# Optimization experiments

Measured on AMD Instinct MI355X. Metric: run time of the kernel, lower is better.

Reference implementation:

```python
import jax, jax.numpy as jnp
import numpy as np

SUBDIVISIONS = 3  # init_kwargs
EPS = 1e-6


def setup_inputs() -> dict:
    key = jax.random.key(0)
    k1, k2, k3 = jax.random.split(key, 3)
    V, K, F = 100000, 32, 64
    features = jax.random.normal(k1, (V, F), dtype=jnp.float32)
    distsq = jax.random.uniform(k2, (V, K), dtype=jnp.float32)
    neighbour_indices = jax.random.randint(k3, (V, K), 0, V, dtype=jnp.int32)
    length_scale = jnp.float32(1.0)  # non-trainable Variable, init 1.0
    return {"features": features, "distsq": distsq,
            "neighbour_indices": neighbour_indices, "length_scale": length_scale}


def reference(features, distsq, neighbour_indices, length_scale):
    # Inference path: no length-scale EMA update (training=None -> in_train_phase takes the
    # unchanged value), distsq is stop-gradient.
    distsq = jax.lax.stop_gradient(distsq)
    scaler = 10.0 * length_scale * float(SUBDIVISIONS)
    d = jnp.sqrt(distsq + EPS)                      # (V, K) neighbor distances
    nfeat = features[neighbour_indices]             # (V, K, F) gathered neighbor features
    outs = []
    for i in range(SUBDIVISIONS):
        offset = float(i) / length_scale            # radius-bin center
        w = jnp.exp(-scaler * (d - offset) ** 2)    # (V, K) Gaussian radius-bin weights
        num = jnp.einsum('vk,vkf->vf', w, nfeat)    # weighted sum over neighbors
        den = jnp.sum(w, axis=1, keepdims=True) + EPS
        outs.append(num / den)                      # soft-pixel weighted mean
    return jnp.concatenate(outs, axis=1)            # (V, SUBDIVISIONS * F)
```

## Files before the change

kernel.cpp:

```cpp
#include <hip/hip_runtime.h>

#define SP_EPS 1e-6f
typedef __fp16 h2 __attribute__((ext_vector_type(2)));
typedef float f32x2 __attribute__((ext_vector_type(2)));

struct __align__(16) QEntry { f32x2 a;  f32x2 b; };

__device__ __forceinline__ f32x2 shflx2(f32x2 x, int m) {
    f32x2 r;
    r.x = __shfl_xor(x.x, m, 64);
    r.y = __shfl_xor(x.y, m, 64);
    return r;
}

__global__ __launch_bounds__(256) void f32_to_f16_kernel(
    const float* __restrict__ in, unsigned* __restrict__ outh, int n4)
{
    int i = blockIdx.x * 256 + threadIdx.x;
    if (i >= n4) return;
    const float4 v = ((const float4*)in)[i];
    h2 p0 = __builtin_amdgcn_cvt_pkrtz(v.x, v.y);
    h2 p1 = __builtin_amdgcn_cvt_pkrtz(v.z, v.w);
    uint2 o;
    o.x = *(unsigned*)&p0;
    o.y = *(unsigned*)&p1;
    ((uint2*)outh)[i] = o;
}

__global__ __launch_bounds__(256) void softpixel_qw_kernel(
    const unsigned short* __restrict__ fb,
    const float* __restrict__ distsq,
    const int*   __restrict__ nidx,
    const float* __restrict__ ls_ptr,
    float*       __restrict__ out,
    int V)
{
    __shared__ QEntry qbuf[4][32];
    const int lane = threadIdx.x & 63;
    const int wv   = threadIdx.x >> 6;
    const int v    = blockIdx.x * 4 + wv;
    const int q    = lane >> 4;
    const int j    = lane & 15;
    const int j32  = lane & 31;
    const int vc   = v < V ? v : V - 1;

    const float ls     = ls_ptr[0];
    const float scaler = 30.0f * ls;
    const float inv_ls = 1.0f / ls;

    const unsigned dvoff = (unsigned)vc * 32u + (unsigned)j32;
    const float dsq = distsq[dvoff];
    const int   nb  = nidx[dvoff];
    const float d   = sqrtf(dsq + SP_EPS);
    const float t1  = d - inv_ls;
    const float t2  = d - 2.0f * inv_ls;
    const float w0  = __expf(-scaler * d  * d);
    const float w1  = __expf(-scaler * t1 * t1);
    const float w2  = __expf(-scaler * t2 * t2);
    if (lane < 32) {
        QEntry e;
        e.a = (f32x2){w0, __int_as_float(nb)};
        e.b = (f32x2){w1, w2};
        qbuf[wv][j32] = e;
    }
    __syncthreads();

    f32x2 a01_0 = {0.f, 0.f}, a23_0 = {0.f, 0.f};
    f32x2 a01_1 = {0.f, 0.f}, a23_1 = {0.f, 0.f};
    f32x2 a01_2 = {0.f, 0.f}, a23_2 = {0.f, 0.f};
    const unsigned j8 = (unsigned)(j << 3);

    #pragma unroll
    for (int kk = 0; kk < 8; ++kk) {
        const QEntry e = qbuf[wv][4 * kk + q];
        const int ik = __float_as_int(e.a.y);
        const unsigned boff = ((unsigned)ik << 7) + j8;
        const uint2 fp = *(const uint2*)((const char*)fb + boff);
        h2 pa, pb;
        *(unsigned*)&pa = fp.x;
        *(unsigned*)&pb = fp.y;
        f32x2 f01; f01.x = (float)pa[0]; f01.y = (float)pa[1];
        f32x2 f23; f23.x = (float)pb[0]; f23.y = (float)pb[1];
        asm("v_pk_fma_f32 %0, %1, %2, %0 op_sel:[0,0,0] op_sel_hi:[0,1,1]"
            : "+v"(a01_0) : "v"(e.a), "v"(f01));
        asm("v_pk_fma_f32 %0, %1, %2, %0 op_sel:[0,0,0] op_sel_hi:[0,1,1]"
            : "+v"(a23_0) : "v"(e.a), "v"(f23));
        asm("v_pk_fma_f32 %0, %1, %2, %0 op_sel:[0,0,0] op_sel_hi:[0,1,1]"
            : "+v"(a01_1) : "v"(e.b), "v"(f01));
        asm("v_pk_fma_f32 %0, %1, %2, %0 op_sel:[0,0,0] op_sel_hi:[0,1,1]"
            : "+v"(a23_1) : "v"(e.b), "v"(f23));
        asm("v_pk_fma_f32 %0, %1, %2, %0 op_sel:[1,0,0] op_sel_hi:[1,1,1]"
            : "+v"(a01_2) : "v"(e.b), "v"(f01));
        asm("v_pk_fma_f32 %0, %1, %2, %0 op_sel:[1,0,0] op_sel_hi:[1,1,1]"
            : "+v"(a23_2) : "v"(e.b), "v"(f23));
    }

    float s0 = w0, s1 = w1, s2 = w2;
    #pragma unroll
    for (int st = 1; st < 32; st <<= 1) {
        s0 += __shfl_xor(s0, st, 64);
        s1 += __shfl_xor(s1, st, 64);
        s2 += __shfl_xor(s2, st, 64);
    }
    const float r0 = __builtin_amdgcn_rcpf(s0 + SP_EPS);
    const float r1 = __builtin_amdgcn_rcpf(s1 + SP_EPS);
    const float r2 = __builtin_amdgcn_rcpf(s2 + SP_EPS);

    a01_0 += shflx2(a01_0, 16);  a01_0 += shflx2(a01_0, 32);
    a23_0 += shflx2(a23_0, 16);  a23_0 += shflx2(a23_0, 32);
    a01_1 += shflx2(a01_1, 16);  a01_1 += shflx2(a01_1, 32);
    a23_1 += shflx2(a23_1, 16);  a23_1 += shflx2(a23_1, 32);
    a01_2 += shflx2(a01_2, 16);  a01_2 += shflx2(a01_2, 32);
    a23_2 += shflx2(a23_2, 16);  a23_2 += shflx2(a23_2, 32);

    if (v < V && q < 3) {
        f32x2 o01, o23;
        float r;
        if (q == 0)      { o01 = a01_0; o23 = a23_0; r = r0; }
        else if (q == 1) { o01 = a01_1; o23 = a23_1; r = r1; }
        else             { o01 = a01_2; o23 = a23_2; r = r2; }
        float4 ov = make_float4(o01.x * r, o01.y * r, o23.x * r, o23.y * r);
        *(float4*)(out + (unsigned)v * 192u + (unsigned)(q << 6) + (unsigned)(j << 2)) = ov;
    }
}

__global__ __launch_bounds__(256) void softpixel_f32_kernel(
    const float* __restrict__ feat,
    const float* __restrict__ distsq,
    const int*   __restrict__ nidx,
    const float* __restrict__ ls_ptr,
    float*       __restrict__ out,
    int V)
{
    const int lane = threadIdx.x & 63;
    const int wv   = threadIdx.x >> 6;
    const int v    = blockIdx.x * 4 + wv;
    if (v >= V) return;

    const float ls     = ls_ptr[0];
    const float scaler = 30.0f * ls;
    const float inv_ls = 1.0f / ls;

    float w0 = 0.f, w1 = 0.f, w2 = 0.f;
    int nb = 0;
    if (lane < 32) {
        const float dsq = distsq[v * 32 + lane];
        nb = nidx[v * 32 + lane];
        const float d  = sqrtf(dsq + SP_EPS);
        const float t1 = d - inv_ls;
        const float t2 = d - 2.0f * inv_ls;
        w0 = __expf(-scaler * d  * d);
        w1 = __expf(-scaler * t1 * t1);
        w2 = __expf(-scaler * t2 * t2);
    }

    float a0 = 0.f, a1 = 0.f, a2 = 0.f;
    float s0 = SP_EPS, s1 = SP_EPS, s2 = SP_EPS;
    #pragma unroll
    for (int k = 0; k < 32; ++k) {
        const int   ik = __shfl(nb, k, 64);
        const float u0 = __shfl(w0, k, 64);
        const float u1 = __shfl(w1, k, 64);
        const float u2 = __shfl(w2, k, 64);
        const float f  = feat[(size_t)ik * 64 + lane];
        a0 = fmaf(u0, f, a0);
        a1 = fmaf(u1, f, a1);
        a2 = fmaf(u2, f, a2);
        s0 += u0; s1 += u1; s2 += u2;
    }
    float* o = out + (size_t)v * 192 + lane;
    o[0]   = a0 / s0;
    o[64]  = a1 / s1;
    o[128] = a2 / s2;
}

extern "C" void kernel_launch(void* const* d_in, const int* in_sizes, int n_in,
                              void* d_out, int out_size, void* d_ws, size_t ws_size,
                              hipStream_t stream) {
    const float* feat   = (const float*)d_in[0];
    const float* distsq = (const float*)d_in[1];
    const int*   nidx   = (const int*)d_in[2];
    const float* ls     = (const float*)d_in[3];

    const int V = in_sizes[1] / 32;
    const int F = in_sizes[0] / V;
    float* out = (float*)d_out;

    const size_t need = (size_t)V * F * sizeof(unsigned short);
    const int grid = (V + 3) / 4;

    if ((size_t)ws_size >= need && F == 64) {
        unsigned* fh = (unsigned*)d_ws;
        const int n4 = V * F / 4;
        f32_to_f16_kernel<<<(n4 + 255) / 256, 256, 0, stream>>>(feat, fh, n4);
        softpixel_qw_kernel<<<grid, 256, 0, stream>>>(
            (const unsigned short*)fh, distsq, nidx, ls, out, V);
    } else {
        softpixel_f32_kernel<<<grid, 256, 0, stream>>>(feat, distsq, nidx, ls, out, V);
    }
}
```

Measured before the change: 74.58 us.

## Process two vertices per wave and replace block barrier with wave barrier

Each 64-lane wave now handles two vertices: both halves compute Gaussian weights for their own vertex, so no lanes sit idle during the weight and exp phase. The gather loop then interleaves two independent feature loads per iteration, giving more memory-level parallelism per wave. The block-wide __syncthreads is replaced by an LDS waitcnt plus a wave barrier, since each wave only reads its own shared slot. In exchange the accumulator count doubles, which raises register pressure and may lower occupancy, and the grid shrinks by half.

```diff
diff --git a/kernel.cpp b/kernel.cpp
--- a/kernel.cpp
+++ b/kernel.cpp
@@ -27,7 +27,7 @@
     ((uint2*)outh)[i] = o;
 }
 
-__global__ __launch_bounds__(256) void softpixel_qw_kernel(
+__global__ __launch_bounds__(256) void softpixel_dual_kernel(
     const unsigned short* __restrict__ fb,
     const float* __restrict__ distsq,
     const int*   __restrict__ nidx,
@@ -35,20 +35,23 @@
     float*       __restrict__ out,
     int V)
 {
-    __shared__ QEntry qbuf[4][32];
+    __shared__ QEntry qbuf[4][64];
     const int lane = threadIdx.x & 63;
     const int wv   = threadIdx.x >> 6;
-    const int v    = blockIdx.x * 4 + wv;
     const int q    = lane >> 4;
     const int j    = lane & 15;
     const int j32  = lane & 31;
-    const int vc   = v < V ? v : V - 1;
+    const int h    = lane >> 5;
+    const int vA   = blockIdx.x * 8 + wv * 2;
+    const int vB   = vA + 1;
+    const int myv  = h ? vB : vA;
+    const int myc  = myv < V ? myv : V - 1;
 
     const float ls     = ls_ptr[0];
     const float scaler = 30.0f * ls;
     const float inv_ls = 1.0f / ls;
 
-    const unsigned dvoff = (unsigned)vc * 32u + (unsigned)j32;
+    const unsigned dvoff = (unsigned)myc * 32u + (unsigned)j32;
     const float dsq = distsq[dvoff];
     const int   nb  = nidx[dvoff];
     const float d   = sqrtf(dsq + SP_EPS);
@@ -57,43 +60,14 @@
     const float w0  = __expf(-scaler * d  * d);
     const float w1  = __expf(-scaler * t1 * t1);
     const float w2  = __expf(-scaler * t2 * t2);
-    if (lane < 32) {
+    {
         QEntry e;
         e.a = (f32x2){w0, __int_as_float(nb)};
         e.b = (f32x2){w1, w2};
-        qbuf[wv][j32] = e;
-    }
-    __syncthreads();
-
-    f32x2 a01_0 = {0.f, 0.f}, a23_0 = {0.f, 0.f};
-    f32x2 a01_1 = {0.f, 0.f}, a23_1 = {0.f, 0.f};
-    f32x2 a01_2 = {0.f, 0.f}, a23_2 = {0.f, 0.f};
-    const unsigned j8 = (unsigned)(j << 3);
-
-    #pragma unroll
-    for (int kk = 0; kk < 8; ++kk) {
-        const QEntry e = qbuf[wv][4 * kk + q];
-        const int ik = __float_as_int(e.a.y);
-        const unsigned boff = ((unsigned)ik << 7) + j8;
-        const uint2 fp = *(const uint2*)((const char*)fb + boff);
-        h2 pa, pb;
-        *(unsigned*)&pa = fp.x;
-        *(unsigned*)&pb = fp.y;
-        f32x2 f01; f01.x = (float)pa[0]; f01.y = (float)pa[1];
-        f32x2 f23; f23.x = (float)pb[0]; f23.y = (float)pb[1];
-        asm("v_pk_fma_f32 %0, %1, %2, %0 op_sel:[0,0,0] op_sel_hi:[0,1,1]"
-            : "+v"(a01_0) : "v"(e.a), "v"(f01));
-        asm("v_pk_fma_f32 %0, %1, %2, %0 op_sel:[0,0,0] op_sel_hi:[0,1,1]"
-            : "+v"(a23_0) : "v"(e.a), "v"(f23));
-        asm("v_pk_fma_f32 %0, %1, %2, %0 op_sel:[0,0,0] op_sel_hi:[0,1,1]"
-            : "+v"(a01_1) : "v"(e.b), "v"(f01));
-        asm("v_pk_fma_f32 %0, %1, %2, %0 op_sel:[0,0,0] op_sel_hi:[0,1,1]"
-            : "+v"(a23_1) : "v"(e.b), "v"(f23));
-        asm("v_pk_fma_f32 %0, %1, %2, %0 op_sel:[1,0,0] op_sel_hi:[1,1,1]"
-            : "+v"(a01_2) : "v"(e.b), "v"(f01));
-        asm("v_pk_fma_f32 %0, %1, %2, %0 op_sel:[1,0,0] op_sel_hi:[1,1,1]"
-            : "+v"(a23_2) : "v"(e.b), "v"(f23));
-    }
+        qbuf[wv][lane] = e;
+    }
+    asm volatile("s_waitcnt lgkmcnt(0)" ::: "memory");
+    __builtin_amdgcn_wave_barrier();
 
     float s0 = w0, s1 = w1, s2 = w2;
     #pragma unroll
@@ -106,21 +80,88 @@
     const float r1 = __builtin_amdgcn_rcpf(s1 + SP_EPS);
     const float r2 = __builtin_amdgcn_rcpf(s2 + SP_EPS);
 
-    a01_0 += shflx2(a01_0, 16);  a01_0 += shflx2(a01_0, 32);
-    a23_0 += shflx2(a23_0, 16);  a23_0 += shflx2(a23_0, 32);
-    a01_1 += shflx2(a01_1, 16);  a01_1 += shflx2(a01_1, 32);
-    a23_1 += shflx2(a23_1, 16);  a23_1 += shflx2(a23_1, 32);
-    a01_2 += shflx2(a01_2, 16);  a01_2 += shflx2(a01_2, 32);
-    a23_2 += shflx2(a23_2, 16);  a23_2 += shflx2(a23_2, 32);
-
-    if (v < V && q < 3) {
-        f32x2 o01, o23;
-        float r;
-        if (q == 0)      { o01 = a01_0; o23 = a23_0; r = r0; }
-        else if (q == 1) { o01 = a01_1; o23 = a23_1; r = r1; }
-        else             { o01 = a01_2; o23 = a23_2; r = r2; }
-        float4 ov = make_float4(o01.x * r, o01.y * r, o23.x * r, o23.y * r);
-        *(float4*)(out + (unsigned)v * 192u + (unsigned)(q << 6) + (unsigned)(j << 2)) = ov;
+    f32x2 a01A_0 = {0.f,0.f}, a23A_0 = {0.f,0.f};
+    f32x2 a01A_1 = {0.f,0.f}, a23A_1 = {0.f,0.f};
+    f32x2 a01A_2 = {0.f,0.f}, a23A_2 = {0.f,0.f};
+    f32x2 a01B_0 = {0.f,0.f}, a23B_0 = {0.f,0.f};
+    f32x2 a01B_1 = {0.f,0.f}, a23B_1 = {0.f,0.f};
+    f32x2 a01B_2 = {0.f,0.f}, a23B_2 = {0.f,0.f};
+    const unsigned j8 = (unsigned)(j << 3);
+
+    #pragma unroll
+    for (int kk = 0; kk < 8; ++kk) {
+        const QEntry eA = qbuf[wv][4 * kk + q];
+        const QEntry eB = qbuf[wv][32 + 4 * kk + q];
+        const unsigned boffA = ((unsigned)__float_as_int(eA.a.y) << 7) + j8;
+        const unsigned boffB = ((unsigned)__float_as_int(eB.a.y) << 7) + j8;
+        const uint2 fpA = *(const uint2*)((const char*)fb + boffA);
+        const uint2 fpB = *(const uint2*)((const char*)fb + boffB);
+        h2 pa, pb;
+        f32x2 f01, f23;
+        *(unsigned*)&pa = fpA.x;  *(unsigned*)&pb = fpA.y;
+        f01.x = (float)pa[0]; f01.y = (float)pa[1];
+        f23.x = (float)pb[0]; f23.y = (float)pb[1];
+        asm("v_pk_fma_f32 %0, %1, %2, %0 op_sel:[0,0,0] op_sel_hi:[0,1,1]"
+            : "+v"(a01A_0) : "v"(eA.a), "v"(f01));
+        asm("v_pk_fma_f32 %0, %1, %2, %0 op_sel:[0,0,0] op_sel_hi:[0,1,1]"
+            : "+v"(a23A_0) : "v"(eA.a), "v"(f23));
+        asm("v_pk_fma_f32 %0, %1, %2, %0 op_sel:[0,0,0] op_sel_hi:[0,1,1]"
+            : "+v"(a01A_1) : "v"(eA.b), "v"(f01));
+        asm("v_pk_fma_f32 %0, %1, %2, %0 op_sel:[0,0,0] op_sel_hi:[0,1,1]"
+            : "+v"(a23A_1) : "v"(eA.b), "v"(f23));
+        asm("v_pk_fma_f32 %0, %1, %2, %0 op_sel:[1,0,0] op_sel_hi:[1,1,1]"
+            : "+v"(a01A_2) : "v"(eA.b), "v"(f01));
+        asm("v_pk_fma_f32 %0, %1, %2, %0 op_sel:[1,0,0] op_sel_hi:[1,1,1]"
+            : "+v"(a23A_2) : "v"(eA.b), "v"(f23));
+        *(unsigned*)&pa = fpB.x;  *(unsigned*)&pb = fpB.y;
+        f01.x = (float)pa[0]; f01.y = (float)pa[1];
+        f23.x = (float)pb[0]; f23.y = (float)pb[1];
+        asm("v_pk_fma_f32 %0, %1, %2, %0 op_sel:[0,0,0] op_sel_hi:[0,1,1]"
+            : "+v"(a01B_0) : "v"(eB.a), "v"(f01));
+        asm("v_pk_fma_f32 %0, %1, %2, %0 op_sel:[0,0,0] op_sel_hi:[0,1,1]"
+            : "+v"(a23B_0) : "v"(eB.a), "v"(f23));
+        asm("v_pk_fma_f32 %0, %1, %2, %0 op_sel:[0,0,0] op_sel_hi:[0,1,1]"
+            : "+v"(a01B_1) : "v"(eB.b), "v"(f01));
+        asm("v_pk_fma_f32 %0, %1, %2, %0 op_sel:[0,0,0] op_sel_hi:[0,1,1]"
+            : "+v"(a23B_1) : "v"(eB.b), "v"(f23));
+        asm("v_pk_fma_f32 %0, %1, %2, %0 op_sel:[1,0,0] op_sel_hi:[1,1,1]"
+            : "+v"(a01B_2) : "v"(eB.b), "v"(f01));
+        asm("v_pk_fma_f32 %0, %1, %2, %0 op_sel:[1,0,0] op_sel_hi:[1,1,1]"
+            : "+v"(a23B_2) : "v"(eB.b), "v"(f23));
+    }
+
+    a01A_0 += shflx2(a01A_0, 16);  a01A_0 += shflx2(a01A_0, 32);
+    a23A_0 += shflx2(a23A_0, 16);  a23A_0 += shflx2(a23A_0, 32);
+    a01A_1 += shflx2(a01A_1, 16);  a01A_1 += shflx2(a01A_1, 32);
+    a23A_1 += shflx2(a23A_1, 16);  a23A_1 += shflx2(a23A_1, 32);
+    a01A_2 += shflx2(a01A_2, 16);  a01A_2 += shflx2(a01A_2, 32);
+    a23A_2 += shflx2(a23A_2, 16);  a23A_2 += shflx2(a23A_2, 32);
+    a01B_0 += shflx2(a01B_0, 16);  a01B_0 += shflx2(a01B_0, 32);
+    a23B_0 += shflx2(a23B_0, 16);  a23B_0 += shflx2(a23B_0, 32);
+    a01B_1 += shflx2(a01B_1, 16);  a01B_1 += shflx2(a01B_1, 32);
+    a23B_1 += shflx2(a23B_1, 16);  a23B_1 += shflx2(a23B_1, 32);
+    a01B_2 += shflx2(a01B_2, 16);  a01B_2 += shflx2(a01B_2, 32);
+    a23B_2 += shflx2(a23B_2, 16);  a23B_2 += shflx2(a23B_2, 32);
+
+    const float rA0 = __shfl(r0, 0, 64),  rA1 = __shfl(r1, 0, 64),  rA2 = __shfl(r2, 0, 64);
+    const float rB0 = __shfl(r0, 32, 64), rB1 = __shfl(r1, 32, 64), rB2 = __shfl(r2, 32, 64);
+
+    if (q < 3) {
+        const float rA = q == 0 ? rA0 : (q == 1 ? rA1 : rA2);
+        const float rB = q == 0 ? rB0 : (q == 1 ? rB1 : rB2);
+        const f32x2 sA01 = q == 0 ? a01A_0 : (q == 1 ? a01A_1 : a01A_2);
+        const f32x2 sA23 = q == 0 ? a23A_0 : (q == 1 ? a23A_1 : a23A_2);
+        const f32x2 sB01 = q == 0 ? a01B_0 : (q == 1 ? a01B_1 : a01B_2);
+        const f32x2 sB23 = q == 0 ? a23B_0 : (q == 1 ? a23B_1 : a23B_2);
+        const unsigned slot = (unsigned)(q << 6) + (unsigned)(j << 2);
+        if (vA < V) {
+            float4 ov = make_float4(sA01.x * rA, sA01.y * rA, sA23.x * rA, sA23.y * rA);
+            *(float4*)(out + (unsigned)vA * 192u + slot) = ov;
+        }
+        if (vB < V) {
+            float4 ov = make_float4(sB01.x * rB, sB01.y * rB, sB23.x * rB, sB23.y * rB);
+            *(float4*)(out + (unsigned)vB * 192u + slot) = ov;
+        }
     }
 }
 
@@ -187,15 +228,16 @@
     float* out = (float*)d_out;
 
     const size_t need = (size_t)V * F * sizeof(unsigned short);
-    const int grid = (V + 3) / 4;
 
     if ((size_t)ws_size >= need && F == 64) {
         unsigned* fh = (unsigned*)d_ws;
         const int n4 = V * F / 4;
         f32_to_f16_kernel<<<(n4 + 255) / 256, 256, 0, stream>>>(feat, fh, n4);
-        softpixel_qw_kernel<<<grid, 256, 0, stream>>>(
+        const int grid = (V + 7) / 8;
+        softpixel_dual_kernel<<<grid, 256, 0, stream>>>(
             (const unsigned short*)fh, distsq, nidx, ls, out, V);
     } else {
+        const int grid = (V + 3) / 4;
         softpixel_f32_kernel<<<grid, 256, 0, stream>>>(feat, distsq, nidx, ls, out, V);
     }
 }
```

New measurement: 74.55 us. About the same (-0.0%).
